# Performance work log

Measured on AMD Instinct MI355X. Metric: run time of the kernel, lower is better.

## Reference

```python
import jax, jax.numpy as jnp
import numpy as np


def setup_inputs() -> dict:
    key = jax.random.key(0)
    ks = jax.random.split(key, 7)
    B, IN, OUT, G = 8192, 2048, 2048, 4
    s_i = 1.0 / np.sqrt(IN)
    s_h = 1.0 / np.sqrt(OUT)
    return {
        "x": jax.random.normal(ks[0], (B, IN), jnp.float32),
        "prev_h": jax.random.normal(ks[1], (B, OUT), jnp.float32),
        "prev_c": jax.random.normal(ks[2], (B, OUT), jnp.float32),
        "Wi": jax.random.normal(ks[3], (G, IN, OUT), jnp.float32) * s_i,
        "Wh": jax.random.normal(ks[4], (G, OUT, OUT), jnp.float32) * s_h,
        "bi": jax.random.normal(ks[5], (G, OUT), jnp.float32) * s_i,
        "bh": jax.random.normal(ks[6], (G, OUT), jnp.float32) * s_h,
    }


def reference(x, prev_h, prev_c, Wi, Wh, bi, bh):
    # Two fused GEMMs replacing 8 per-gate Linears (gate order: in, forget, in2, out)
    # gates: [B, 4, OUT]
    gates = (jnp.einsum("bi,gio->bgo", x, Wi) + bi[None]
             + jnp.einsum("bh,gho->bgo", prev_h, Wh) + bh[None])
    in_gate = jax.nn.sigmoid(gates[:, 0])
    forget_gate = jax.nn.sigmoid(gates[:, 1])
    in_gate2 = jax.nn.sigmoid(gates[:, 2])
    out_gate = jax.nn.sigmoid(gates[:, 3])
    next_c = forget_gate * prev_c + in_gate * in_gate2
    # NOTE: faithful to source: out_gate + tanh(next_c) (addition, not multiply)
    next_h = out_gate + jnp.tanh(next_c)
    return next_h, next_c
```

## Files before the change

kernel.cpp:

```cpp
#include <hip/hip_runtime.h>
#include <stdint.h>


#define SZ_ELEMS 16777216
#define HALF_OUT 16777216

typedef __attribute__((ext_vector_type(8))) short bf16x8;
typedef __attribute__((ext_vector_type(4))) float f32x4;
typedef __attribute__((ext_vector_type(8))) unsigned short u16x8;

__device__ __forceinline__ unsigned short f2bf(float f) {
  unsigned int u = __float_as_uint(f);
  u += 0x7FFFu + ((u >> 16) & 1u);
  return (unsigned short)(u >> 16);
}

__device__ __forceinline__ void async16(const void* g, void* l) {
  __builtin_amdgcn_global_load_lds(
      (const __attribute__((address_space(1))) void*)g,
      (__attribute__((address_space(3))) void*)l, 16, 0, 0);
}

__device__ __forceinline__ float sigm(float x) { return 1.f / (1.f + __expf(-x)); }

__global__ void cvt_bf16_kernel(const float* __restrict__ src,
                                unsigned short* __restrict__ dst, int n4) {
  int i = blockIdx.x * blockDim.x + threadIdx.x;
  int stride = gridDim.x * blockDim.x;
  for (; i < n4; i += stride) {
    float4 v = reinterpret_cast<const float4*>(src)[i];
    ushort4 o;
    o.x = f2bf(v.x); o.y = f2bf(v.y); o.z = f2bf(v.z); o.w = f2bf(v.w);
    reinterpret_cast<ushort4*>(dst)[i] = o;
  }
}

__global__ void transpose_w_kernel(const float* __restrict__ Wi, const float* __restrict__ Wh,
                                   unsigned short* __restrict__ Wit, unsigned short* __restrict__ Wht) {
  __shared__ float tile[64][65];
  const int tk = blockIdx.x, to = blockIdx.y, gz = blockIdx.z;
  const float* W = (gz < 4 ? Wi : Wh) + (size_t)(gz & 3) * 4194304;
  unsigned short* Wt = (gz < 4 ? Wit : Wht) + (size_t)(gz & 3) * 4194304;
  const int t = threadIdx.x;
  const int o = t & 63, kr = t >> 6;
#pragma unroll
  for (int p = 0; p < 16; ++p) {
    int k = p * 4 + kr;
    tile[k][o] = W[(size_t)(tk * 64 + k) * 2048 + to * 64 + o];
  }
  __syncthreads();
#pragma unroll
  for (int p = 0; p < 2; ++p) {
    int idx = p * 256 + t;
    int orow = idx >> 3, k0 = (idx & 7) * 8;
    u16x8 v;
#pragma unroll
    for (int i = 0; i < 8; ++i) v[i] = f2bf(tile[k0 + i][orow]);
    *reinterpret_cast<u16x8*>(&Wt[(size_t)(to * 64 + orow) * 2048 + tk * 64 + k0]) = v;
  }
}

__global__ __launch_bounds__(256, 2) void lstm_gemm_kernel(
    const unsigned short* __restrict__ xb, const unsigned short* __restrict__ hb,
    const unsigned short* __restrict__ wit, const unsigned short* __restrict__ wht,
    const float* __restrict__ bi, const float* __restrict__ bh,
    const float* __restrict__ prev_c, float* __restrict__ out) {
  __shared__ uint4 lds_u[49152 / 16];
  char* lds = (char*)lds_u;
  char* ldsA = lds;
  char* ldsB = lds + 16384;

  const int tid = threadIdx.x;
  const int wave = tid >> 6, lane = tid & 63;
  const int wm = wave >> 1, wn = wave & 1;
  const int bm = blockIdx.x;
  const int bo = blockIdx.y;

  int aoff[4]; char* adst[4];
#pragma unroll
  for (int j = 0; j < 4; ++j) {
    int L = (wave * 4 + j) * 1024 + lane * 16;
    int row = L >> 7;
    int kb = (L & 127) ^ ((row & 7) << 4);
    aoff[j] = row * 4096 + kb;
    adst[j] = ldsA + (wave * 4 + j) * 1024;
  }
  int boff[8]; char* bdst[8];
#pragma unroll
  for (int j = 0; j < 8; ++j) {
    int L = (wave * 8 + j) * 1024 + lane * 16;
    int g = L >> 13;
    int rem = L & 8191;
    int row = rem >> 7;
    int kb = (rem & 127) ^ ((row & 7) << 4);
    boff[j] = g * 8388608 + row * 4096 + kb;
    bdst[j] = ldsB + (wave * 8 + j) * 1024;
  }

  const char* aBase0 = (const char*)xb + (size_t)bm * 128 * 4096;
  const char* aBase1 = (const char*)hb + (size_t)bm * 128 * 4096;
  const char* bBase0 = (const char*)wit + (size_t)bo * 64 * 4096;
  const char* bBase1 = (const char*)wht + (size_t)bo * 64 * 4096;

  f32x4 acc[4][4][2];
  const f32x4 zero = {0.f, 0.f, 0.f, 0.f};
#pragma unroll
  for (int g = 0; g < 4; ++g)
#pragma unroll
    for (int mf = 0; mf < 4; ++mf)
#pragma unroll
      for (int nf = 0; nf < 2; ++nf) acc[g][mf][nf] = zero;

  for (int s = 0; s < 64; ++s) {
    const char* ab = (s < 32) ? (aBase0 + s * 128) : (aBase1 + (s - 32) * 128);
    const char* bb = (s < 32) ? (bBase0 + s * 128) : (bBase1 + (s - 32) * 128);
#pragma unroll
    for (int j = 0; j < 4; ++j) async16(ab + aoff[j], adst[j]);
#pragma unroll
    for (int j = 0; j < 8; ++j) async16(bb + boff[j], bdst[j]);
    __syncthreads();

#pragma unroll
    for (int ks = 0; ks < 2; ++ks) {
      const int kb = ks * 64 + ((lane >> 4) << 4);
      const int swz = (lane & 7) << 4;
      bf16x8 afr[4];
#pragma unroll
      for (int mf = 0; mf < 4; ++mf) {
        int row = wm * 64 + mf * 16 + (lane & 15);
        afr[mf] = *(const bf16x8*)(ldsA + row * 128 + (kb ^ swz));
      }
#pragma unroll
      for (int g = 0; g < 4; ++g) {
#pragma unroll
        for (int nf = 0; nf < 2; ++nf) {
          int row = wn * 32 + nf * 16 + (lane & 15);
          bf16x8 bfr = *(const bf16x8*)(ldsB + g * 8192 + row * 128 + (kb ^ swz));
#pragma unroll
          for (int mf = 0; mf < 4; ++mf)
            acc[g][mf][nf] = __builtin_amdgcn_mfma_f32_16x16x32_bf16(afr[mf], bfr, acc[g][mf][nf], 0, 0, 0);
        }
      }
    }
    __syncthreads();
  }

  const int col = lane & 15, rg = lane >> 4;
#pragma unroll
  for (int nf = 0; nf < 2; ++nf) {
    int o = bo * 64 + wn * 32 + nf * 16 + col;
    float bs0 = bi[o] + bh[o];
    float bs1 = bi[2048 + o] + bh[2048 + o];
    float bs2 = bi[4096 + o] + bh[4096 + o];
    float bs3 = bi[6144 + o] + bh[6144 + o];
#pragma unroll
    for (int mf = 0; mf < 4; ++mf) {
      int bbase = bm * 128 + wm * 64 + mf * 16 + rg * 4;
#pragma unroll
      for (int r = 0; r < 4; ++r) {
        int b = bbase + r;
        float gi = sigm(acc[0][mf][nf][r] + bs0);
        float gf = sigm(acc[1][mf][nf][r] + bs1);
        float g2 = sigm(acc[2][mf][nf][r] + bs2);
        float go = sigm(acc[3][mf][nf][r] + bs3);
        float c = prev_c[(size_t)b * 2048 + o];
        float nc = gf * c + gi * g2;
        float e = __expf(2.f * nc);
        float nh = go + (e - 1.f) / (e + 1.f);
        out[(size_t)b * 2048 + o] = nh;
        out[(size_t)HALF_OUT + (size_t)b * 2048 + o] = nc;
      }
    }
  }
}

extern "C" void kernel_launch(void* const* d_in, const int* in_sizes, int n_in,
                              void* d_out, int out_size, void* d_ws, size_t ws_size,
                              hipStream_t stream) {
  const float* x  = (const float*)d_in[0];
  const float* ph = (const float*)d_in[1];
  const float* pc = (const float*)d_in[2];
  const float* Wi = (const float*)d_in[3];
  const float* Wh = (const float*)d_in[4];
  const float* bi = (const float*)d_in[5];
  const float* bh = (const float*)d_in[6];
  float* out = (float*)d_out;

  if (ws_size < (size_t)4 * SZ_ELEMS * sizeof(unsigned short)) return;
  unsigned short* xb  = (unsigned short*)d_ws;
  unsigned short* hb  = xb + SZ_ELEMS;
  unsigned short* wit = hb + SZ_ELEMS;
  unsigned short* wht = wit + SZ_ELEMS;

  cvt_bf16_kernel<<<2048, 256, 0, stream>>>(x, xb, 4194304);
  cvt_bf16_kernel<<<2048, 256, 0, stream>>>(ph, hb, 4194304);
  transpose_w_kernel<<<dim3(32, 32, 8), 256, 0, stream>>>(Wi, Wh, wit, wht);
  lstm_gemm_kernel<<<dim3(64, 32), 256, 0, stream>>>(xb, hb, wit, wht, bi, bh, pc, out);
}
```

Measured before the change: 584.6 us.

## Enlarge GEMM tile to 256x256 with 8 waves and double-buffered async LDS loads

```diff
diff --git a/kernel.cpp b/kernel.cpp
--- a/kernel.cpp
+++ b/kernel.cpp
@@ -60,116 +60,121 @@
   }
 }
 
-__global__ __launch_bounds__(256, 2) void lstm_gemm_kernel(
+__global__ __launch_bounds__(512, 2) void lstm_gemm_kernel(
     const unsigned short* __restrict__ xb, const unsigned short* __restrict__ hb,
     const unsigned short* __restrict__ wit, const unsigned short* __restrict__ wht,
     const float* __restrict__ bi, const float* __restrict__ bh,
     const float* __restrict__ prev_c, float* __restrict__ out) {
-  __shared__ uint4 lds_u[49152 / 16];
-  char* lds = (char*)lds_u;
-  char* ldsA = lds;
-  char* ldsB = lds + 16384;
+  __shared__ char lds[131072];
 
   const int tid = threadIdx.x;
   const int wave = tid >> 6, lane = tid & 63;
-  const int wm = wave >> 1, wn = wave & 1;
+  const int wm = wave >> 2, wn = wave & 3;
   const int bm = blockIdx.x;
   const int bo = blockIdx.y;
 
-  int aoff[4]; char* adst[4];
+  int aoff[4], boff[4];
 #pragma unroll
   for (int j = 0; j < 4; ++j) {
-    int L = (wave * 4 + j) * 1024 + lane * 16;
-    int row = L >> 7;
-    int kb = (L & 127) ^ ((row & 7) << 4);
-    aoff[j] = row * 4096 + kb;
-    adst[j] = ldsA + (wave * 4 + j) * 1024;
-  }
-  int boff[8]; char* bdst[8];
-#pragma unroll
-  for (int j = 0; j < 8; ++j) {
-    int L = (wave * 8 + j) * 1024 + lane * 16;
-    int g = L >> 13;
-    int rem = L & 8191;
-    int row = rem >> 7;
-    int kb = (rem & 127) ^ ((row & 7) << 4);
-    boff[j] = g * 8388608 + row * 4096 + kb;
-    bdst[j] = ldsB + (wave * 8 + j) * 1024;
-  }
-
-  const char* aBase0 = (const char*)xb + (size_t)bm * 128 * 4096;
-  const char* aBase1 = (const char*)hb + (size_t)bm * 128 * 4096;
-  const char* bBase0 = (const char*)wit + (size_t)bo * 64 * 4096;
-  const char* bBase1 = (const char*)wht + (size_t)bo * 64 * 4096;
-
-  f32x4 acc[4][4][2];
+    int L = j * 8192 + tid * 16;
+    int row = L >> 7, c = L & 127;
+    aoff[j] = row * 4096 + (c ^ ((row & 7) << 4));
+    boff[j] = (row >> 6) * 8388608 + (row & 63) * 4096 + (c ^ ((row & 7) << 4));
+  }
+  const int ldst = tid * 16;
+
+  const char* aB0 = (const char*)xb + (size_t)bm * 1048576;
+  const char* aB1 = (const char*)hb + (size_t)bm * 1048576;
+  const char* bB0 = (const char*)wit + (size_t)bo * 262144;
+  const char* bB1 = (const char*)wht + (size_t)bo * 262144;
+
+  auto stage = [&](int s, int buf) {
+    const char* ab; const char* bb;
+    if (s < 32) { ab = aB0 + s * 128;        bb = bB0 + s * 128; }
+    else        { ab = aB1 + (s - 32) * 128; bb = bB1 + (s - 32) * 128; }
+    char* l = lds + buf * 65536;
+#pragma unroll
+    for (int j = 0; j < 4; ++j) async16(ab + aoff[j], l + j * 8192 + ldst);
+#pragma unroll
+    for (int j = 0; j < 4; ++j) async16(bb + boff[j], l + 32768 + j * 8192 + ldst);
+  };
+
+  f32x4 acc[8][4];
   const f32x4 zero = {0.f, 0.f, 0.f, 0.f};
 #pragma unroll
-  for (int g = 0; g < 4; ++g)
-#pragma unroll
-    for (int mf = 0; mf < 4; ++mf)
-#pragma unroll
-      for (int nf = 0; nf < 2; ++nf) acc[g][mf][nf] = zero;
-
-  for (int s = 0; s < 64; ++s) {
-    const char* ab = (s < 32) ? (aBase0 + s * 128) : (aBase1 + (s - 32) * 128);
-    const char* bb = (s < 32) ? (bBase0 + s * 128) : (bBase1 + (s - 32) * 128);
-#pragma unroll
-    for (int j = 0; j < 4; ++j) async16(ab + aoff[j], adst[j]);
-#pragma unroll
-    for (int j = 0; j < 8; ++j) async16(bb + boff[j], bdst[j]);
-    __syncthreads();
-
+  for (int mf = 0; mf < 8; ++mf)
+#pragma unroll
+    for (int nf = 0; nf < 4; ++nf) acc[mf][nf] = zero;
+
+  const int kwin = (lane >> 4) << 4;
+  const int swz  = (lane & 7) << 4;
+  int aro[8], bro[4];
+#pragma unroll
+  for (int mf = 0; mf < 8; ++mf) aro[mf] = (wm * 128 + mf * 16 + (lane & 15)) * 128;
+#pragma unroll
+  for (int nf = 0; nf < 4; ++nf) bro[nf] = 32768 + (nf * 64 + wn * 16 + (lane & 15)) * 128;
+
+  auto compute = [&](int buf) {
+    const char* l = lds + buf * 65536;
 #pragma unroll
     for (int ks = 0; ks < 2; ++ks) {
-      const int kb = ks * 64 + ((lane >> 4) << 4);
-      const int swz = (lane & 7) << 4;
-      bf16x8 afr[4];
-#pragma unroll
-      for (int mf = 0; mf < 4; ++mf) {
-        int row = wm * 64 + mf * 16 + (lane & 15);
-        afr[mf] = *(const bf16x8*)(ldsA + row * 128 + (kb ^ swz));
-      }
-#pragma unroll
-      for (int g = 0; g < 4; ++g) {
-#pragma unroll
-        for (int nf = 0; nf < 2; ++nf) {
-          int row = wn * 32 + nf * 16 + (lane & 15);
-          bf16x8 bfr = *(const bf16x8*)(ldsB + g * 8192 + row * 128 + (kb ^ swz));
-#pragma unroll
-          for (int mf = 0; mf < 4; ++mf)
-            acc[g][mf][nf] = __builtin_amdgcn_mfma_f32_16x16x32_bf16(afr[mf], bfr, acc[g][mf][nf], 0, 0, 0);
-        }
+      const int kb = (ks * 64 + kwin) ^ swz;
+      bf16x8 afr[8];
+#pragma unroll
+      for (int mf = 0; mf < 8; ++mf) afr[mf] = *(const bf16x8*)(l + aro[mf] + kb);
+#pragma unroll
+      for (int nf = 0; nf < 4; ++nf) {
+        bf16x8 bfr = *(const bf16x8*)(l + bro[nf] + kb);
+#pragma unroll
+        for (int mf = 0; mf < 8; ++mf)
+          acc[mf][nf] = __builtin_amdgcn_mfma_f32_16x16x32_bf16(afr[mf], bfr, acc[mf][nf], 0, 0, 0);
       }
     }
-    __syncthreads();
-  }
+  };
+
+  stage(0, 0);
+  for (int t = 0; t < 63; ++t) {
+    asm volatile("" ::: "memory");
+    __builtin_amdgcn_s_barrier();
+    asm volatile("" ::: "memory");
+    stage(t + 1, (t + 1) & 1);
+    asm volatile("s_waitcnt vmcnt(8)" ::: "memory");
+    __builtin_amdgcn_s_barrier();
+    asm volatile("" ::: "memory");
+    __builtin_amdgcn_s_setprio(1);
+    compute(t & 1);
+    __builtin_amdgcn_s_setprio(0);
+  }
+  asm volatile("" ::: "memory");
+  __builtin_amdgcn_s_barrier();
+  asm volatile("s_waitcnt vmcnt(0)" ::: "memory");
+  __builtin_amdgcn_s_barrier();
+  asm volatile("" ::: "memory");
+  __builtin_amdgcn_s_setprio(1);
+  compute(1);
+  __builtin_amdgcn_s_setprio(0);
 
   const int col = lane & 15, rg = lane >> 4;
-#pragma unroll
-  for (int nf = 0; nf < 2; ++nf) {
-    int o = bo * 64 + wn * 32 + nf * 16 + col;
-    float bs0 = bi[o] + bh[o];
-    float bs1 = bi[2048 + o] + bh[2048 + o];
-    float bs2 = bi[4096 + o] + bh[4096 + o];
-    float bs3 = bi[6144 + o] + bh[6144 + o];
-#pragma unroll
-    for (int mf = 0; mf < 4; ++mf) {
-      int bbase = bm * 128 + wm * 64 + mf * 16 + rg * 4;
-#pragma unroll
-      for (int r = 0; r < 4; ++r) {
-        int b = bbase + r;
-        float gi = sigm(acc[0][mf][nf][r] + bs0);
-        float gf = sigm(acc[1][mf][nf][r] + bs1);
-        float g2 = sigm(acc[2][mf][nf][r] + bs2);
-        float go = sigm(acc[3][mf][nf][r] + bs3);
-        float c = prev_c[(size_t)b * 2048 + o];
-        float nc = gf * c + gi * g2;
-        float e = __expf(2.f * nc);
-        float nh = go + (e - 1.f) / (e + 1.f);
-        out[(size_t)b * 2048 + o] = nh;
-        out[(size_t)HALF_OUT + (size_t)b * 2048 + o] = nc;
-      }
+  const int o = bo * 64 + wn * 16 + col;
+  float bs[4];
+#pragma unroll
+  for (int g = 0; g < 4; ++g) bs[g] = bi[g * 2048 + o] + bh[g * 2048 + o];
+#pragma unroll
+  for (int mf = 0; mf < 8; ++mf) {
+    int bbase = bm * 256 + wm * 128 + mf * 16 + rg * 4;
+#pragma unroll
+    for (int r = 0; r < 4; ++r) {
+      int b = bbase + r;
+      float gi = sigm(acc[mf][0][r] + bs[0]);
+      float gf = sigm(acc[mf][1][r] + bs[1]);
+      float g2 = sigm(acc[mf][2][r] + bs[2]);
+      float go = sigm(acc[mf][3][r] + bs[3]);
+      float c = prev_c[(size_t)b * 2048 + o];
+      float nc = gf * c + gi * g2;
+      float e = __expf(2.f * nc);
+      float nh = go + (e - 1.f) / (e + 1.f);
+      out[(size_t)b * 2048 + o] = nh;
+      out[(size_t)HALF_OUT + (size_t)b * 2048 + o] = nc;
     }
   }
 }
@@ -195,5 +200,5 @@
   cvt_bf16_kernel<<<2048, 256, 0, stream>>>(x, xb, 4194304);
   cvt_bf16_kernel<<<2048, 256, 0, stream>>>(ph, hb, 4194304);
   transpose_w_kernel<<<dim3(32, 32, 8), 256, 0, stream>>>(Wi, Wh, wit, wht);
-  lstm_gemm_kernel<<<dim3(64, 32), 256, 0, stream>>>(xb, hb, wit, wht, bi, bh, pc, out);
-}
+  lstm_gemm_kernel<<<dim3(32, 32), 512, 0, stream>>>(xb, hb, wit, wht, bi, bh, pc, out);
+}
```

Result: faster. 556.7 us (-4.8%).
